# Performance work log

Measured on AMD Instinct MI355X. Metric: run time of the kernel, lower is better.

Reference implementation:

```python
import jax, jax.numpy as jnp
import numpy as np

SIGMA = 100.0
M = 64
N_DIMS = 3
XH_IN = 9           # n_dims + in_node_nf + context_node_nf
XH_HID = 64         # xh_hidden_size
POS_HID = 192       # hidden_size - xh_hidden_size
TWO_PI = 2.0 * np.pi


def setup_inputs() -> dict:
    key = jax.random.key(0)
    ks = jax.random.split(key, 6)
    B, N = 8, 256
    t = jax.random.uniform(ks[0], (B, 1), dtype=jnp.float32)
    xh = jax.random.normal(ks[1], (B, N, XH_IN), dtype=jnp.float32)
    node_mask = jnp.ones((B, N, 1), dtype=jnp.float32)
    edge_mask = jnp.ones((B, N * N, 1), dtype=jnp.float32)
    # learned params: xh_embedder Linear(9->64), pos_embedder Linear(2m->192)
    W_xh = jax.random.normal(ks[2], (XH_IN, XH_HID), dtype=jnp.float32) / np.sqrt(XH_IN)
    b_xh = jnp.zeros((XH_HID,), dtype=jnp.float32)
    W_pos = jax.random.normal(ks[3], (2 * M, POS_HID), dtype=jnp.float32) / np.sqrt(2 * M)
    b_pos = jnp.zeros((POS_HID,), dtype=jnp.float32)
    return {"t": t, "xh": xh, "node_mask": node_mask, "edge_mask": edge_mask,
            "W_xh": W_xh, "b_xh": b_xh, "W_pos": W_pos, "b_pos": b_pos}


def remove_mean_with_mask(x, node_mask, N):
    # masked mean over node axis, re-masked output
    mean = jnp.sum(x * node_mask, axis=1, keepdims=True) / N  # [B,1,3]
    return (x - mean) * node_mask


def positional_encoding(d, sigma, m):
    # d: [B,N,N,1] -> Fourier features [B,N,N,2m] with geometric freqs sigma^(j/m)
    freqs = sigma ** (jnp.arange(m, dtype=jnp.float32) / m)  # [m]
    ang = TWO_PI * d * freqs                                  # [B,N,N,m]
    return jnp.concatenate([jnp.sin(ang), jnp.cos(ang)], axis=-1)


def reference(t, xh, node_mask, edge_mask, W_xh, b_xh, W_pos, b_pos):
    x = xh[..., :N_DIMS]
    h = xh[..., N_DIMS:]
    N = jnp.sum(node_mask, axis=1, keepdims=True)  # [B,1,1]
    x = remove_mean_with_mask(x, node_mask, N)
    # node feature embedding: [B,N,64]
    xh_emb = jnp.concatenate([x, h], axis=-1) @ W_xh + b_xh
    # pairwise distances (safe sqrt for diagonal zeros)
    diff = x[:, :, None, :] - x[:, None, :, :]                 # [B,N,N,3]
    sq = jnp.maximum(jnp.sum(diff * diff, axis=-1), 0.0)
    dist = jnp.sqrt(sq + 1e-12)                                # [B,N,N]
    pe = positional_encoding(dist[..., None], SIGMA, M)        # [B,N,N,2m]
    pe = pe * node_mask[:, :, :, None] * node_mask[:, None, :, :]
    pe = (pe @ W_pos + b_pos)                                  # [B,N,N,192]
    pe = jnp.sum(pe, axis=-2) / N                              # [B,N,192]
    out = jnp.concatenate([xh_emb, pe], axis=-1) * node_mask   # [B,N,256]
    return out
```

## Files before the change

kernel.cpp:

```cpp
#include <hip/hip_runtime.h>
#include <math.h>

#define BB 8
#define NN 256
#define XHIN 9
#define XHHID 64
#define POSHID 192
#define RPB 4

__global__ __launch_bounds__(256) void mean_kernel(
    const float* __restrict__ xh, const float* __restrict__ mask,
    float* __restrict__ ws_xc, float* __restrict__ ws_cnt)
{
  const int b = blockIdx.x;
  const int n = threadIdx.x;

  const float* p = xh + (b * NN + n) * XHIN;
  const float x0 = p[0], x1 = p[1], x2 = p[2];
  const float m = mask[b * NN + n];

  float a0 = x0 * m, a1 = x1 * m, a2 = x2 * m, a3 = m;
  #pragma unroll
  for (int off = 32; off > 0; off >>= 1) {
    a0 += __shfl_down(a0, off, 64);
    a1 += __shfl_down(a1, off, 64);
    a2 += __shfl_down(a2, off, 64);
    a3 += __shfl_down(a3, off, 64);
  }
  __shared__ float red[4][4];
  const int lane = n & 63, wv = n >> 6;
  if (lane == 0) { red[wv][0] = a0; red[wv][1] = a1; red[wv][2] = a2; red[wv][3] = a3; }
  __syncthreads();

  const float s0 = red[0][0] + red[1][0] + red[2][0] + red[3][0];
  const float s1 = red[0][1] + red[1][1] + red[2][1] + red[3][1];
  const float s2 = red[0][2] + red[1][2] + red[2][2] + red[3][2];
  const float cnt = red[0][3] + red[1][3] + red[2][3] + red[3][3];
  const float inv = 1.0f / cnt;

  ws_xc[(b * 3 + 0) * NN + n] = (x0 - s0 * inv) * m;
  ws_xc[(b * 3 + 1) * NN + n] = (x1 - s1 * inv) * m;
  ws_xc[(b * 3 + 2) * NN + n] = (x2 - s2 * inv) * m;
  if (n == 0) ws_cnt[b] = cnt;
}

__global__ __launch_bounds__(256) void sfield_kernel(
    const float* __restrict__ ws_xc, const float* __restrict__ ws_cnt,
    const float* __restrict__ mask, float* __restrict__ ws_S)
{
  const int blk = blockIdx.x;
  const int b = blk >> 8;
  const int i = blk & 255;
  const int tid = threadIdx.x;

  __shared__ float2 dm_s[NN];
  __shared__ float part[4][128];

  const float* xcb = ws_xc + b * 3 * NN;
  const float xi0 = xcb[0 * NN + i];
  const float xi1 = xcb[1 * NN + i];
  const float xi2 = xcb[2 * NN + i];
  {
    const int j = tid;
    const float dx = xi0 - xcb[0 * NN + j];
    const float dy = xi1 - xcb[1 * NN + j];
    const float dz = xi2 - xcb[2 * NN + j];
    const float sq = fmaf(dx, dx, fmaf(dy, dy, dz * dz));
    dm_s[j] = make_float2(sqrtf(sq + 1e-12f), mask[b * NN + j]);
  }
  __syncthreads();

  const int f = tid & 63, jg = tid >> 6;
  const float freq = __builtin_exp2f((float)f * 0.10381025296523007f);
  float ss = 0.f, cc = 0.f;
  const float2* dmp = dm_s + jg * 64;
  #pragma unroll 16
  for (int u = 0; u < 64; ++u) {
    const float2 dm = dmp[u];
    const float rv = __builtin_amdgcn_fractf(dm.x * freq);
    ss = fmaf(__builtin_amdgcn_sinf(rv), dm.y, ss);
    cc = fmaf(__builtin_amdgcn_cosf(rv), dm.y, cc);
  }
  part[jg][f] = ss;
  part[jg][64 + f] = cc;
  __syncthreads();

  if (tid < 128) {
    const float cnt = ws_cnt[b];
    const float mi = dm_s[i].y;
    ws_S[(size_t)blk * 128 + tid] =
        (part[0][tid] + part[1][tid] + part[2][tid] + part[3][tid]) * (mi / cnt);
  }
}

__global__ __launch_bounds__(256) void out_kernel(
    const float* __restrict__ ws_S, const float* __restrict__ ws_xc,
    const float* __restrict__ ws_cnt, const float* __restrict__ mask,
    const float* __restrict__ xh,
    const float* __restrict__ Wxh, const float* __restrict__ bxh,
    const float* __restrict__ Wp, const float* __restrict__ bp,
    float* __restrict__ out)
{
  const int blk = blockIdx.x;
  const int row0 = blk * RPB;
  const int b = row0 >> 8;
  const int i0 = row0 & 255;
  const int tid = threadIdx.x;

  __shared__ __align__(16) float S_l[RPB][128];
  __shared__ float ins_l[RPB][XHIN];
  __shared__ float Wxh_l[XHIN * XHHID];
  __shared__ float bxh_l[XHHID];
  __shared__ float bscale_l[RPB];
  __shared__ float mi_l[RPB];

  if (tid < 128)
    ((float4*)S_l)[tid] = ((const float4*)(ws_S + (size_t)row0 * 128))[tid];
  if (tid < 192) {
    Wxh_l[tid]       = Wxh[tid];
    Wxh_l[tid + 192] = Wxh[tid + 192];
    Wxh_l[tid + 384] = Wxh[tid + 384];
  }
  if (tid < XHHID) bxh_l[tid] = bxh[tid];
  if (tid < RPB * XHIN) {
    const int r = tid / XHIN, k = tid % XHIN;
    const int i = i0 + r;
    ins_l[r][k] = (k < 3) ? ws_xc[(b * 3 + k) * NN + i]
                          : xh[(size_t)(b * NN + i) * XHIN + k];
  }
  if (tid < RPB) {
    const float m = mask[b * NN + i0 + tid];
    mi_l[tid] = m;
    bscale_l[tid] = m * 256.0f / ws_cnt[b];
  }
  __syncthreads();

  if (tid < POSHID) {
    const int col = tid;
    float acc[RPB];
    #pragma unroll
    for (int r = 0; r < RPB; ++r) acc[r] = bp[col] * bscale_l[r];

    #pragma unroll 8
    for (int k4 = 0; k4 < 32; ++k4) {
      const float* w = Wp + (k4 * 4) * POSHID + col;
      const float w0 = w[0 * POSHID];
      const float w1 = w[1 * POSHID];
      const float w2 = w[2 * POSHID];
      const float w3 = w[3 * POSHID];
      #pragma unroll
      for (int r = 0; r < RPB; ++r) {
        const float4 s = ((const float4*)S_l[r])[k4];
        acc[r] = fmaf(s.w, w3, fmaf(s.z, w2, fmaf(s.y, w1, fmaf(s.x, w0, acc[r]))));
      }
    }
    #pragma unroll
    for (int r = 0; r < RPB; ++r)
      out[(size_t)(row0 + r) * 256 + 64 + col] = acc[r];
  } else {
    const int oo = tid - POSHID;
    #pragma unroll
    for (int r = 0; r < RPB; ++r) {
      float acc = bxh_l[oo];
      #pragma unroll
      for (int k = 0; k < XHIN; ++k)
        acc = fmaf(ins_l[r][k], Wxh_l[k * XHHID + oo], acc);
      out[(size_t)(row0 + r) * 256 + oo] = acc * mi_l[r];
    }
  }
}

extern "C" void kernel_launch(void* const* d_in, const int* in_sizes, int n_in,
                              void* d_out, int out_size, void* d_ws, size_t ws_size,
                              hipStream_t stream) {
  const float* xh   = (const float*)d_in[1];
  const float* mask = (const float*)d_in[2];
  const float* Wxh  = (const float*)d_in[4];
  const float* bxh  = (const float*)d_in[5];
  const float* Wp   = (const float*)d_in[6];
  const float* bp   = (const float*)d_in[7];
  float* out = (float*)d_out;

  float* ws_xc  = (float*)d_ws;
  float* ws_cnt = ws_xc + BB * 3 * NN;
  float* ws_S   = ws_cnt + 64;

  mean_kernel<<<BB, 256, 0, stream>>>(xh, mask, ws_xc, ws_cnt);
  sfield_kernel<<<BB * NN, 256, 0, stream>>>(ws_xc, ws_cnt, mask, ws_S);
  out_kernel<<<BB * NN / RPB, 256, 0, stream>>>(ws_S, ws_xc, ws_cnt, mask, xh,
                                                Wxh, bxh, Wp, bp, out);
}
```

Measured before the change: 85.60 us.

## Exploit distance symmetry with upper-triangular tile pairs and atomic accumulation

The per-row sin/cos field kernel is replaced by a tiled kernel that only processes upper-triangular 16x16 tile pairs. Each computed sin/cos value is accumulated into both the row and the column sums, which roughly halves the transcendental work. Results go into a zero-initialised global buffer through atomics, with the zeroing folded into the mean kernel. The mask/count scaling moves to the output kernel. The cost is many global float atomics and shared-memory atomics, plus a reduction order that is no longer deterministic.

```diff
diff --git a/kernel.cpp b/kernel.cpp
--- a/kernel.cpp
+++ b/kernel.cpp
@@ -6,12 +6,24 @@
 #define XHIN 9
 #define XHHID 64
 #define POSHID 192
+#define TS 16
+#define NT (NN / TS)
+#define NPAIR (NT * (NT + 1) / 2)
 #define RPB 4
-
-__global__ __launch_bounds__(256) void mean_kernel(
+#define FREQC 0.10381025296523007f
+
+__global__ __launch_bounds__(256) void mean_zero_kernel(
     const float* __restrict__ xh, const float* __restrict__ mask,
-    float* __restrict__ ws_xc, float* __restrict__ ws_cnt)
+    float* __restrict__ ws_xc, float* __restrict__ ws_cnt,
+    float4* __restrict__ ws_S4)
 {
+  if (blockIdx.x >= BB) {
+    const int base = (blockIdx.x - BB) * 1024 + threadIdx.x;
+    #pragma unroll
+    for (int k = 0; k < 4; ++k)
+      ws_S4[base + k * 256] = make_float4(0.f, 0.f, 0.f, 0.f);
+    return;
+  }
   const int b = blockIdx.x;
   const int n = threadIdx.x;
 
@@ -44,52 +56,111 @@
   if (n == 0) ws_cnt[b] = cnt;
 }
 
-__global__ __launch_bounds__(256) void sfield_kernel(
-    const float* __restrict__ ws_xc, const float* __restrict__ ws_cnt,
-    const float* __restrict__ mask, float* __restrict__ ws_S)
+__global__ __launch_bounds__(256) void pairs_kernel(
+    const float* __restrict__ ws_xc, const float* __restrict__ mask,
+    float* __restrict__ ws_S)
 {
-  const int blk = blockIdx.x;
-  const int b = blk >> 8;
-  const int i = blk & 255;
+  const int b = blockIdx.x / NPAIR;
+  int p = blockIdx.x % NPAIR;
+  int I = 0;
+  while (p >= NT - I) { p -= NT - I; ++I; }
+  const int J = I + p;
+  const bool diag = (I == J);
   const int tid = threadIdx.x;
 
-  __shared__ float2 dm_s[NN];
-  __shared__ float part[4][128];
-
-  const float* xcb = ws_xc + b * 3 * NN;
-  const float xi0 = xcb[0 * NN + i];
-  const float xi1 = xcb[1 * NN + i];
-  const float xi2 = xcb[2 * NN + i];
+  __shared__ float xs[2][3][TS];
+  __shared__ float ms[2][TS];
+  __shared__ __align__(16) float d_s[TS][TS];
+  __shared__ float Sj[TS][128];
+
+  if (tid < 96) {
+    const int t = tid / 48, r = tid % 48, c = r / 16, n = r % 16;
+    xs[t][c][n] = ws_xc[(b * 3 + c) * NN + (t ? J : I) * TS + n];
+  }
+  if (tid < 32) {
+    const int t = tid >> 4, n = tid & 15;
+    ms[t][n] = mask[b * NN + (t ? J : I) * TS + n];
+  }
   {
-    const int j = tid;
-    const float dx = xi0 - xcb[0 * NN + j];
-    const float dy = xi1 - xcb[1 * NN + j];
-    const float dz = xi2 - xcb[2 * NN + j];
-    const float sq = fmaf(dx, dx, fmaf(dy, dy, dz * dz));
-    dm_s[j] = make_float2(sqrtf(sq + 1e-12f), mask[b * NN + j]);
-  }
-  __syncthreads();
-
-  const int f = tid & 63, jg = tid >> 6;
-  const float freq = __builtin_exp2f((float)f * 0.10381025296523007f);
-  float ss = 0.f, cc = 0.f;
-  const float2* dmp = dm_s + jg * 64;
-  #pragma unroll 16
-  for (int u = 0; u < 64; ++u) {
-    const float2 dm = dmp[u];
-    const float rv = __builtin_amdgcn_fractf(dm.x * freq);
-    ss = fmaf(__builtin_amdgcn_sinf(rv), dm.y, ss);
-    cc = fmaf(__builtin_amdgcn_cosf(rv), dm.y, cc);
-  }
-  part[jg][f] = ss;
-  part[jg][64 + f] = cc;
-  __syncthreads();
-
-  if (tid < 128) {
-    const float cnt = ws_cnt[b];
-    const float mi = dm_s[i].y;
-    ws_S[(size_t)blk * 128 + tid] =
-        (part[0][tid] + part[1][tid] + part[2][tid] + part[3][tid]) * (mi / cnt);
+    float4* z = (float4*)Sj;
+    z[tid] = make_float4(0.f, 0.f, 0.f, 0.f);
+    z[tid + 256] = make_float4(0.f, 0.f, 0.f, 0.f);
+  }
+  __syncthreads();
+  {
+    const int i = tid & 15, j = tid >> 4;
+    const float dx = xs[0][0][i] - xs[1][0][j];
+    const float dy = xs[0][1][i] - xs[1][1][j];
+    const float dz = xs[0][2][i] - xs[1][2][j];
+    d_s[j][i] = sqrtf(fmaf(dx, dx, fmaf(dy, dy, dz * dz)) + 1e-12f);
+  }
+  __syncthreads();
+
+  const int f = tid & 63, g = tid >> 6;
+  const float freq = __builtin_exp2f((float)f * FREQC);
+  float si0 = 0.f, si1 = 0.f, si2 = 0.f, si3 = 0.f;
+  float ci0 = 0.f, ci1 = 0.f, ci2 = 0.f, ci3 = 0.f;
+  const float mA0 = ms[0][g * 4 + 0], mA1 = ms[0][g * 4 + 1];
+  const float mA2 = ms[0][g * 4 + 2], mA3 = ms[0][g * 4 + 3];
+
+  #pragma unroll 4
+  for (int j = 0; j < TS; ++j) {
+    const float4 d4 = *(const float4*)&d_s[j][g * 4];
+    const float mj = ms[1][j];
+    float sj = 0.f, cj = 0.f;
+    {
+      const float rv = __builtin_amdgcn_fractf(d4.x * freq);
+      const float s_ = __builtin_amdgcn_sinf(rv);
+      const float c_ = __builtin_amdgcn_cosf(rv);
+      si0 = fmaf(mj, s_, si0); ci0 = fmaf(mj, c_, ci0);
+      sj = fmaf(mA0, s_, sj);  cj = fmaf(mA0, c_, cj);
+    }
+    {
+      const float rv = __builtin_amdgcn_fractf(d4.y * freq);
+      const float s_ = __builtin_amdgcn_sinf(rv);
+      const float c_ = __builtin_amdgcn_cosf(rv);
+      si1 = fmaf(mj, s_, si1); ci1 = fmaf(mj, c_, ci1);
+      sj = fmaf(mA1, s_, sj);  cj = fmaf(mA1, c_, cj);
+    }
+    {
+      const float rv = __builtin_amdgcn_fractf(d4.z * freq);
+      const float s_ = __builtin_amdgcn_sinf(rv);
+      const float c_ = __builtin_amdgcn_cosf(rv);
+      si2 = fmaf(mj, s_, si2); ci2 = fmaf(mj, c_, ci2);
+      sj = fmaf(mA2, s_, sj);  cj = fmaf(mA2, c_, cj);
+    }
+    {
+      const float rv = __builtin_amdgcn_fractf(d4.w * freq);
+      const float s_ = __builtin_amdgcn_sinf(rv);
+      const float c_ = __builtin_amdgcn_cosf(rv);
+      si3 = fmaf(mj, s_, si3); ci3 = fmaf(mj, c_, ci3);
+      sj = fmaf(mA3, s_, sj);  cj = fmaf(mA3, c_, cj);
+    }
+    if (!diag) {
+      atomicAdd(&Sj[j][f], sj);
+      atomicAdd(&Sj[j][64 + f], cj);
+    }
+  }
+
+  {
+    const int row = b * NN + I * TS + g * 4;
+    atomicAdd(&ws_S[(size_t)(row + 0) * 128 + f], si0);
+    atomicAdd(&ws_S[(size_t)(row + 0) * 128 + 64 + f], ci0);
+    atomicAdd(&ws_S[(size_t)(row + 1) * 128 + f], si1);
+    atomicAdd(&ws_S[(size_t)(row + 1) * 128 + 64 + f], ci1);
+    atomicAdd(&ws_S[(size_t)(row + 2) * 128 + f], si2);
+    atomicAdd(&ws_S[(size_t)(row + 2) * 128 + 64 + f], ci2);
+    atomicAdd(&ws_S[(size_t)(row + 3) * 128 + f], si3);
+    atomicAdd(&ws_S[(size_t)(row + 3) * 128 + 64 + f], ci3);
+  }
+  if (!diag) {
+    __syncthreads();
+    #pragma unroll
+    for (int k = 0; k < 8; ++k) {
+      const int idx = k * 256 + tid;
+      const int j = idx >> 7, ff = idx & 127;
+      atomicAdd(&ws_S[(size_t)(b * NN + J * TS + j) * 128 + ff], Sj[j][ff]);
+    }
   }
 }
 
@@ -111,6 +182,7 @@
   __shared__ float ins_l[RPB][XHIN];
   __shared__ float Wxh_l[XHIN * XHHID];
   __shared__ float bxh_l[XHHID];
+  __shared__ float scl_l[RPB];
   __shared__ float bscale_l[RPB];
   __shared__ float mi_l[RPB];
 
@@ -130,16 +202,19 @@
   }
   if (tid < RPB) {
     const float m = mask[b * NN + i0 + tid];
+    const float cnt = ws_cnt[b];
     mi_l[tid] = m;
-    bscale_l[tid] = m * 256.0f / ws_cnt[b];
+    scl_l[tid] = m / cnt;
+    bscale_l[tid] = m * 256.0f / cnt;
   }
   __syncthreads();
 
   if (tid < POSHID) {
     const int col = tid;
+    const float bpc = bp[col];
     float acc[RPB];
     #pragma unroll
-    for (int r = 0; r < RPB; ++r) acc[r] = bp[col] * bscale_l[r];
+    for (int r = 0; r < RPB; ++r) acc[r] = 0.f;
 
     #pragma unroll 8
     for (int k4 = 0; k4 < 32; ++k4) {
@@ -156,7 +231,7 @@
     }
     #pragma unroll
     for (int r = 0; r < RPB; ++r)
-      out[(size_t)(row0 + r) * 256 + 64 + col] = acc[r];
+      out[(size_t)(row0 + r) * 256 + 64 + col] = acc[r] * scl_l[r] + bpc * bscale_l[r];
   } else {
     const int oo = tid - POSHID;
     #pragma unroll
@@ -185,8 +260,9 @@
   float* ws_cnt = ws_xc + BB * 3 * NN;
   float* ws_S   = ws_cnt + 64;
 
-  mean_kernel<<<BB, 256, 0, stream>>>(xh, mask, ws_xc, ws_cnt);
-  sfield_kernel<<<BB * NN, 256, 0, stream>>>(ws_xc, ws_cnt, mask, ws_S);
+  mean_zero_kernel<<<BB + 64, 256, 0, stream>>>(xh, mask, ws_xc, ws_cnt,
+                                                (float4*)ws_S);
+  pairs_kernel<<<BB * NPAIR, 256, 0, stream>>>(ws_xc, mask, ws_S);
   out_kernel<<<BB * NN / RPB, 256, 0, stream>>>(ws_S, ws_xc, ws_cnt, mask, xh,
                                                 Wxh, bxh, Wp, bp, out);
 }
```

After: 132.5 us. 1.55x slower.

## Exploit distance symmetry with triangular tile pairs and partial-sum reduction

Applied to the files above, without the earlier changes.

Replaces the per-row Fourier-feature kernel with a kernel over upper-triangular 16x16 tile pairs. Each pair's sin/cos values are computed once and accumulated both along rows and, through wave shuffles, along columns, so the transcendental work is roughly halved. Per-tile partial sums go to a much larger workspace, which the output kernel reduces across 16 tiles before the projection GEMM; that GEMM now reads interleaved sin/cos. The cost is far more workspace write/read traffic, extra shuffles, and a different floating-point summation order.

```diff
diff --git a/kernel.cpp b/kernel.cpp
--- a/kernel.cpp
+++ b/kernel.cpp
@@ -6,7 +6,11 @@
 #define XHIN 9
 #define XHHID 64
 #define POSHID 192
-#define RPB 4
+#define TS 16
+#define NT (NN / TS)
+#define NPAIR (NT * (NT + 1) / 2)
+#define RPB 2
+#define FREQC 0.10381025296523007f
 
 __global__ __launch_bounds__(256) void mean_kernel(
     const float* __restrict__ xh, const float* __restrict__ mask,
@@ -44,57 +48,100 @@
   if (n == 0) ws_cnt[b] = cnt;
 }
 
-__global__ __launch_bounds__(256) void sfield_kernel(
-    const float* __restrict__ ws_xc, const float* __restrict__ ws_cnt,
-    const float* __restrict__ mask, float* __restrict__ ws_S)
+__global__ __launch_bounds__(256) void pairs_kernel(
+    const float* __restrict__ ws_xc, const float* __restrict__ mask,
+    float* __restrict__ ws_P)
 {
-  const int blk = blockIdx.x;
-  const int b = blk >> 8;
-  const int i = blk & 255;
+  const int b = blockIdx.x / NPAIR;
+  int p = blockIdx.x % NPAIR;
+  int I = 0;
+  while (p >= NT - I) { p -= NT - I; ++I; }
+  const int J = I + p;
+  const bool diag = (I == J);
   const int tid = threadIdx.x;
 
-  __shared__ float2 dm_s[NN];
-  __shared__ float part[4][128];
-
-  const float* xcb = ws_xc + b * 3 * NN;
-  const float xi0 = xcb[0 * NN + i];
-  const float xi1 = xcb[1 * NN + i];
-  const float xi2 = xcb[2 * NN + i];
+  __shared__ float xs[2][3][TS];
+  __shared__ float msk[2][TS];
+  __shared__ __align__(16) float d_s[TS][TS];
+
+  if (tid < 96) {
+    const int t = tid / 48, r = tid % 48, c = r / 16, n = r % 16;
+    xs[t][c][n] = ws_xc[(b * 3 + c) * NN + (t ? J : I) * TS + n];
+  }
+  if (tid < 32) {
+    const int t = tid >> 4, n = tid & 15;
+    msk[t][n] = mask[b * NN + (t ? J : I) * TS + n];
+  }
+  __syncthreads();
   {
-    const int j = tid;
-    const float dx = xi0 - xcb[0 * NN + j];
-    const float dy = xi1 - xcb[1 * NN + j];
-    const float dz = xi2 - xcb[2 * NN + j];
-    const float sq = fmaf(dx, dx, fmaf(dy, dy, dz * dz));
-    dm_s[j] = make_float2(sqrtf(sq + 1e-12f), mask[b * NN + j]);
-  }
-  __syncthreads();
-
-  const int f = tid & 63, jg = tid >> 6;
-  const float freq = __builtin_exp2f((float)f * 0.10381025296523007f);
-  float ss = 0.f, cc = 0.f;
-  const float2* dmp = dm_s + jg * 64;
-  #pragma unroll 16
-  for (int u = 0; u < 64; ++u) {
-    const float2 dm = dmp[u];
-    const float rv = __builtin_amdgcn_fractf(dm.x * freq);
-    ss = fmaf(__builtin_amdgcn_sinf(rv), dm.y, ss);
-    cc = fmaf(__builtin_amdgcn_cosf(rv), dm.y, cc);
-  }
-  part[jg][f] = ss;
-  part[jg][64 + f] = cc;
-  __syncthreads();
-
-  if (tid < 128) {
-    const float cnt = ws_cnt[b];
-    const float mi = dm_s[i].y;
-    ws_S[(size_t)blk * 128 + tid] =
-        (part[0][tid] + part[1][tid] + part[2][tid] + part[3][tid]) * (mi / cnt);
+    const int i = tid & 15, j = tid >> 4;
+    const float dx = xs[0][0][i] - xs[1][0][j];
+    const float dy = xs[0][1][i] - xs[1][1][j];
+    const float dz = xs[0][2][i] - xs[1][2][j];
+    d_s[j][i] = sqrtf(fmaf(dx, dx, fmaf(dy, dy, dz * dz)) + 1e-12f);
+  }
+  __syncthreads();
+
+  const int g = tid & 3;
+  const int f = tid >> 2;
+  const float freq = __builtin_exp2f((float)f * FREQC);
+
+  float si0 = 0.f, si1 = 0.f, si2 = 0.f, si3 = 0.f;
+  float ci0 = 0.f, ci1 = 0.f, ci2 = 0.f, ci3 = 0.f;
+  float js0, js1, js2, js3, jc0, jc1, jc2, jc3;
+  const float mA0 = msk[0][g * 4 + 0], mA1 = msk[0][g * 4 + 1];
+  const float mA2 = msk[0][g * 4 + 2], mA3 = msk[0][g * 4 + 3];
+
+  #pragma unroll
+  for (int j = 0; j < TS; ++j) {
+    const float4 d4 = *(const float4*)&d_s[j][g * 4];
+    const float mj = msk[1][j];
+    const float r0 = __builtin_amdgcn_fractf(d4.x * freq);
+    const float r1 = __builtin_amdgcn_fractf(d4.y * freq);
+    const float r2 = __builtin_amdgcn_fractf(d4.z * freq);
+    const float r3 = __builtin_amdgcn_fractf(d4.w * freq);
+    const float s0 = __builtin_amdgcn_sinf(r0), c0 = __builtin_amdgcn_cosf(r0);
+    const float s1 = __builtin_amdgcn_sinf(r1), c1 = __builtin_amdgcn_cosf(r1);
+    const float s2 = __builtin_amdgcn_sinf(r2), c2 = __builtin_amdgcn_cosf(r2);
+    const float s3 = __builtin_amdgcn_sinf(r3), c3 = __builtin_amdgcn_cosf(r3);
+    si0 = fmaf(mj, s0, si0); ci0 = fmaf(mj, c0, ci0);
+    si1 = fmaf(mj, s1, si1); ci1 = fmaf(mj, c1, ci1);
+    si2 = fmaf(mj, s2, si2); ci2 = fmaf(mj, c2, ci2);
+    si3 = fmaf(mj, s3, si3); ci3 = fmaf(mj, c3, ci3);
+
+    float sj = fmaf(mA0, s0, fmaf(mA1, s1, fmaf(mA2, s2, mA3 * s3)));
+    float cj = fmaf(mA0, c0, fmaf(mA1, c1, fmaf(mA2, c2, mA3 * c3)));
+    sj += __shfl_xor(sj, 1, 64); sj += __shfl_xor(sj, 2, 64);
+    cj += __shfl_xor(cj, 1, 64); cj += __shfl_xor(cj, 2, 64);
+    if ((j & 3) == g) {
+      const int u = j >> 2;
+      if (u == 0) { js0 = sj; jc0 = cj; }
+      else if (u == 1) { js1 = sj; jc1 = cj; }
+      else if (u == 2) { js2 = sj; jc2 = cj; }
+      else { js3 = sj; jc3 = cj; }
+    }
+  }
+
+  {
+    float2* dst = (float2*)(ws_P +
+        ((size_t)(b * NT + J) * NN + I * TS + g * 4) * 128);
+    dst[0 * 64 + f] = make_float2(si0, ci0);
+    dst[1 * 64 + f] = make_float2(si1, ci1);
+    dst[2 * 64 + f] = make_float2(si2, ci2);
+    dst[3 * 64 + f] = make_float2(si3, ci3);
+  }
+  if (!diag) {
+    float2* dst = (float2*)(ws_P +
+        ((size_t)(b * NT + I) * NN + J * TS) * 128);
+    dst[(size_t)(4 * 0 + g) * 64 + f] = make_float2(js0, jc0);
+    dst[(size_t)(4 * 1 + g) * 64 + f] = make_float2(js1, jc1);
+    dst[(size_t)(4 * 2 + g) * 64 + f] = make_float2(js2, jc2);
+    dst[(size_t)(4 * 3 + g) * 64 + f] = make_float2(js3, jc3);
   }
 }
 
 __global__ __launch_bounds__(256) void out_kernel(
-    const float* __restrict__ ws_S, const float* __restrict__ ws_xc,
+    const float* __restrict__ ws_P, const float* __restrict__ ws_xc,
     const float* __restrict__ ws_cnt, const float* __restrict__ mask,
     const float* __restrict__ xh,
     const float* __restrict__ Wxh, const float* __restrict__ bxh,
@@ -111,11 +158,20 @@
   __shared__ float ins_l[RPB][XHIN];
   __shared__ float Wxh_l[XHIN * XHHID];
   __shared__ float bxh_l[XHHID];
+  __shared__ float scl_l[RPB];
   __shared__ float bscale_l[RPB];
   __shared__ float mi_l[RPB];
 
-  if (tid < 128)
-    ((float4*)S_l)[tid] = ((const float4*)(ws_S + (size_t)row0 * 128))[tid];
+  {
+    const int r = tid >> 7, c = tid & 127;
+    const int i = i0 + r;
+    const float* src = ws_P + (size_t)b * NT * NN * 128 + (size_t)i * 128 + c;
+    float s = 0.f;
+    #pragma unroll
+    for (int T = 0; T < NT; ++T)
+      s += src[(size_t)T * NN * 128];
+    S_l[r][c] = s;
+  }
   if (tid < 192) {
     Wxh_l[tid]       = Wxh[tid];
     Wxh_l[tid + 192] = Wxh[tid + 192];
@@ -130,33 +186,33 @@
   }
   if (tid < RPB) {
     const float m = mask[b * NN + i0 + tid];
+    const float cnt = ws_cnt[b];
     mi_l[tid] = m;
-    bscale_l[tid] = m * 256.0f / ws_cnt[b];
+    scl_l[tid] = m / cnt;
+    bscale_l[tid] = m * 256.0f / cnt;
   }
   __syncthreads();
 
   if (tid < POSHID) {
     const int col = tid;
-    float acc[RPB];
-    #pragma unroll
-    for (int r = 0; r < RPB; ++r) acc[r] = bp[col] * bscale_l[r];
+    const float bpc = bp[col];
+    float acc0 = 0.f, acc1 = 0.f;
 
     #pragma unroll 8
-    for (int k4 = 0; k4 < 32; ++k4) {
-      const float* w = Wp + (k4 * 4) * POSHID + col;
-      const float w0 = w[0 * POSHID];
-      const float w1 = w[1 * POSHID];
-      const float w2 = w[2 * POSHID];
-      const float w3 = w[3 * POSHID];
-      #pragma unroll
-      for (int r = 0; r < RPB; ++r) {
-        const float4 s = ((const float4*)S_l[r])[k4];
-        acc[r] = fmaf(s.w, w3, fmaf(s.z, w2, fmaf(s.y, w1, fmaf(s.x, w0, acc[r]))));
-      }
+    for (int u = 0; u < 32; ++u) {
+      const float4 s0 = ((const float4*)S_l[0])[u];
+      const float4 s1 = ((const float4*)S_l[1])[u];
+      const float* wA = Wp + (2 * u) * POSHID + col;
+      const float* wB = Wp + (64 + 2 * u) * POSHID + col;
+      const float w0 = wA[0];
+      const float w1 = wB[0];
+      const float w2 = wA[POSHID];
+      const float w3 = wB[POSHID];
+      acc0 = fmaf(s0.w, w3, fmaf(s0.z, w2, fmaf(s0.y, w1, fmaf(s0.x, w0, acc0))));
+      acc1 = fmaf(s1.w, w3, fmaf(s1.z, w2, fmaf(s1.y, w1, fmaf(s1.x, w0, acc1))));
     }
-    #pragma unroll
-    for (int r = 0; r < RPB; ++r)
-      out[(size_t)(row0 + r) * 256 + 64 + col] = acc[r];
+    out[(size_t)(row0 + 0) * 256 + 64 + col] = acc0 * scl_l[0] + bpc * bscale_l[0];
+    out[(size_t)(row0 + 1) * 256 + 64 + col] = acc1 * scl_l[1] + bpc * bscale_l[1];
   } else {
     const int oo = tid - POSHID;
     #pragma unroll
@@ -183,10 +239,10 @@
 
   float* ws_xc  = (float*)d_ws;
   float* ws_cnt = ws_xc + BB * 3 * NN;
-  float* ws_S   = ws_cnt + 64;
+  float* ws_P   = ws_cnt + 64;
 
   mean_kernel<<<BB, 256, 0, stream>>>(xh, mask, ws_xc, ws_cnt);
-  sfield_kernel<<<BB * NN, 256, 0, stream>>>(ws_xc, ws_cnt, mask, ws_S);
-  out_kernel<<<BB * NN / RPB, 256, 0, stream>>>(ws_S, ws_xc, ws_cnt, mask, xh,
+  pairs_kernel<<<BB * NPAIR, 256, 0, stream>>>(ws_xc, mask, ws_P);
+  out_kernel<<<BB * NN / RPB, 256, 0, stream>>>(ws_P, ws_xc, ws_cnt, mask, xh,
                                                 Wxh, bxh, Wp, bp, out);
 }
```

Result: slower. 95.58 us (+11.7%).
